# Kernel optimization log

Hardware: AMD Instinct MI355X
Metric: run time of the kernel (lower is better)

Reference implementation:

```python
import jax, jax.numpy as jnp
import numpy as np

B, N, M = 16, 4096, 1024
INPUT_DIM, COND_DIM = 512, 512
HEADS, DIM_HEAD = 8, 64
HIDDEN = HEADS * DIM_HEAD


def setup_inputs() -> dict:
    key = jax.random.key(0)
    ks = jax.random.split(key, 6)
    x = jax.random.normal(ks[0], (B, INPUT_DIM, N), dtype=jnp.float32)
    c = jax.random.normal(ks[1], (B, COND_DIM, M), dtype=jnp.float32)
    # 1x1 conv weights as [out_ch, in_ch] matrices
    Wq = jax.random.normal(ks[2], (HIDDEN, INPUT_DIM), dtype=jnp.float32) * (INPUT_DIM ** -0.5)
    Wkv = jax.random.normal(ks[3], (2 * HIDDEN, COND_DIM), dtype=jnp.float32) * (COND_DIM ** -0.5)
    Wo = jax.random.normal(ks[4], (INPUT_DIM, HIDDEN), dtype=jnp.float32) * (HIDDEN ** -0.5)
    bo = jax.random.normal(ks[5], (INPUT_DIM,), dtype=jnp.float32) * 0.01
    return {"x": x, "c": c, "Wq": Wq, "Wkv": Wkv, "Wo": Wo, "bo": bo}


def reference(x, c, Wq, Wkv, Wo, bo):
    scale = DIM_HEAD ** -0.5
    # 1x1 convs == channel-mixing matmuls
    q = jnp.einsum('bcn,oc->bon', x, Wq)            # [B, HIDDEN, N]
    kv = jnp.einsum('bcm,oc->bom', c, Wkv)          # [B, 2*HIDDEN, M]
    k, v = jnp.split(kv, 2, axis=1)                 # each [B, HIDDEN, M]
    # split heads: b (h d) n -> b h d n
    q = q.reshape(B, HEADS, DIM_HEAD, N) * scale
    k = k.reshape(B, HEADS, DIM_HEAD, M)
    v = v.reshape(B, HEADS, DIM_HEAD, M)
    # softmax over conditioning sequence dim
    k = jax.nn.softmax(k, axis=-1)
    # context: [B, H, d, e] (dim_head x dim_head)
    context = jnp.einsum('bhdm,bhem->bhde', k, v)
    # out: [B, H, e, N]
    out = jnp.einsum('bhde,bhdn->bhen', context, q)
    out = out.reshape(B, HIDDEN, N)
    return jnp.einsum('bcn,oc->bon', out, Wo) + bo[None, :, None]
```

## Files before the change

kernel.cpp:

```cpp
#include <hip/hip_runtime.h>

#define KDIM 512

typedef __attribute__((ext_vector_type(8))) short bf16x8;
typedef __attribute__((ext_vector_type(4))) float f32x4;
typedef unsigned short u16;
typedef unsigned int u32;

static __device__ __forceinline__ u16 f2bf(float f) {
  u32 u = __builtin_bit_cast(u32, f);
  u32 r = u + 0x7fffu + ((u >> 16) & 1u);
  return (u16)(r >> 16);
}
static __device__ __forceinline__ bf16x8 ld_frag(const u16* p) {
  uint2 lo = *(const uint2*)p;
  uint2 hi = *(const uint2*)(p + 4);
  uint4 u = make_uint4(lo.x, lo.y, hi.x, hi.y);
  return __builtin_bit_cast(bf16x8, u);
}

__global__ __launch_bounds__(256) void cvt_f32_bf16(
    const float* __restrict__ src, u16* __restrict__ dst, int n8)
{
  int i = blockIdx.x * 256 + threadIdx.x;
  if (i >= n8) return;
  float4 a = *(const float4*)(src + (long)i * 8);
  float4 b = *(const float4*)(src + (long)i * 8 + 4);
  u32 w0 = (u32)f2bf(a.x) | ((u32)f2bf(a.y) << 16);
  u32 w1 = (u32)f2bf(a.z) | ((u32)f2bf(a.w) << 16);
  u32 w2 = (u32)f2bf(b.x) | ((u32)f2bf(b.y) << 16);
  u32 w3 = (u32)f2bf(b.z) | ((u32)f2bf(b.w) << 16);
  *(uint4*)(dst + (long)i * 8) = make_uint4(w0, w1, w2, w3);
}

#define A0OFF 0
#define A1OFF 18432
#define B0OFF 36864
#define B1OFF 41472

#define P_LOADA(pa, kt) { _Pragma("unroll") \
  for (int i_ = 0; i_ < 4; ++i_) \
    pa[i_] = *(const uint4*)(Ab + (long)(arow + i_ * 128) * KDIM + (kt) + ac * 8); }

#define P_LOADB(q0, q1, kt) { \
  q0 = *(const float4*)(Bb + (long)((kt) + krow)     * ldn + nq * 4); \
  q1 = *(const float4*)(Bb + (long)((kt) + krow + 1) * ldn + nq * 4); }

#define P_STAGE(pa, q0, q1, ab, bb) { \
  _Pragma("unroll") for (int i_ = 0; i_ < 4; ++i_) { \
    u16* d_ = &lds[(ab) + (arow + i_ * 128) * 36 + ac * 8]; \
    *(uint2*)d_       = make_uint2(pa[i_].x, pa[i_].y); \
    *(uint2*)(d_ + 4) = make_uint2(pa[i_].z, pa[i_].w); } \
  float f0_[4] = {q0.x, q0.y, q0.z, q0.w}; \
  float f1_[4] = {q1.x, q1.y, q1.z, q1.w}; \
  _Pragma("unroll") for (int j_ = 0; j_ < 4; ++j_) { \
    u32 w_ = (u32)f2bf(f0_[j_]) | ((u32)f2bf(f1_[j_]) << 16); \
    *(u32*)&lds[(bb) + (nq * 4 + j_) * 36 + krow] = w_; } }

#define P_MFMA(ab, bb) { \
  bf16x8 bfr_[4]; \
  _Pragma("unroll") for (int ni_ = 0; ni_ < 4; ++ni_) \
    bfr_[ni_] = ld_frag(&lds[(bb) + (wn * 64 + ni_ * 16 + lrow) * 36 + lkh * 8]); \
  __builtin_amdgcn_s_setprio(1); \
  _Pragma("unroll") for (int mi_ = 0; mi_ < 8; ++mi_) { \
    bf16x8 af_ = ld_frag(&lds[(ab) + (wm * 128 + mi_ * 16 + lrow) * 36 + lkh * 8]); \
    _Pragma("unroll") for (int ni_ = 0; ni_ < 4; ++ni_) \
      acc[mi_][ni_] = __builtin_amdgcn_mfma_f32_16x16x32_bf16(af_, bfr_[ni_], acc[mi_][ni_], 0, 0, 0); } \
  __builtin_amdgcn_s_setprio(0); }

template<bool OUT_BF16, bool BIAS, int MT, int NT>
__global__ __launch_bounds__(512, 2) void gemm_p(
    const u16* __restrict__ Ap, long a_bstride,
    const float* __restrict__ Bp, long b_bstride,
    void* __restrict__ Op, long o_bstride,
    const float* __restrict__ bias, int ldn)
{
  __shared__ u16 lds[46080];

  const int d = blockIdx.x;
  const int mt = d % MT;
  const int nt = (d / MT) % NT;
  const int b  = d / (MT * NT);
  const long mtile = (long)mt * 512;
  const long ntile = (long)nt * 128;
  const u16* Ab = Ap + (long)b * a_bstride + mtile * KDIM;
  const float* Bb = Bp + (long)b * b_bstride + ntile;

  const int t = threadIdx.x;
  const int lane = t & 63, wv = t >> 6;
  const int wm = wv >> 1, wn = wv & 1;
  const int lrow = lane & 15, lkh = lane >> 4;

  const int arow = t >> 2, ac = t & 3;
  const int nq = t & 31;
  const int hi = (t >> 8) & 1;
  const int kq = ((t >> 5) & 7) ^ ((t >> 2) & 7);
  const int krow = kq * 4 + hi * 2;

  f32x4 acc[8][4] = {};
  uint4 pa0[4], pa1[4];
  float4 b0a, b0b, b1a, b1b;

  P_LOADA(pa0, 0)  P_LOADB(b0a, b0b, 0)
  P_LOADA(pa1, 32) P_LOADB(b1a, b1b, 32)
  P_STAGE(pa0, b0a, b0b, A0OFF, B0OFF)
  __syncthreads();

  for (int s2 = 0; s2 < 8; ++s2) {
    const int kt = s2 * 64;
    if (s2 < 7) { P_LOADA(pa0, kt + 64) P_LOADB(b0a, b0b, kt + 64) }
    P_MFMA(A0OFF, B0OFF)
    P_STAGE(pa1, b1a, b1b, A1OFF, B1OFF)
    __syncthreads();
    if (s2 < 7) { P_LOADA(pa1, kt + 96) P_LOADB(b1a, b1b, kt + 96) }
    P_MFMA(A1OFF, B1OFF)
    if (s2 < 7) {
      P_STAGE(pa0, b0a, b0b, A0OFF, B0OFF)
      __syncthreads();
    }
  }

  #pragma unroll
  for (int mi = 0; mi < 8; ++mi) {
    #pragma unroll
    for (int r = 0; r < 4; ++r) {
      long gr = mtile + wm * 128 + mi * 16 + lkh * 4 + r;
      float bv = 0.0f;
      if constexpr (BIAS) bv = bias[gr];
      #pragma unroll
      for (int ni = 0; ni < 4; ++ni) {
        long gc = ntile + wn * 64 + ni * 16 + lrow;
        float v = acc[mi][ni][r] + bv;
        if constexpr (OUT_BF16)
          ((u16*)Op)[(long)b * o_bstride + gr * ldn + gc] = f2bf(v);
        else
          ((float*)Op)[(long)b * o_bstride + gr * ldn + gc] = v;
      }
    }
  }
}

__global__ __launch_bounds__(256, 2) void softmax_context(
    const u16* __restrict__ kv, float* __restrict__ ctx)
{
  constexpr int LDE = 132;
  __shared__ float rowmax[64], rowinv[64];
  __shared__ u16 Ke[64 * LDE];
  __shared__ u16 Vs[64 * LDE];
  __shared__ float pr[64 * 68];

  const int bh = blockIdx.x;
  const u16* Kr = kv + (long)(bh >> 3) * (1024 * 1024) + (long)(bh & 7) * (64 * 1024);
  const u16* Vr = Kr + 512 * 1024;

  const int t = threadIdx.x;
  const int lane = t & 63, wv = t >> 6;
  const int lrow = lane & 15, lkh = lane >> 4;
  const int d4 = t >> 2, q4 = t & 3;

  {
    const u16* row = Kr + d4 * 1024 + q4 * 256;
    float mx = -3e38f;
    for (int i = 0; i < 256; i += 8) {
      uint4 v = *(const uint4*)(row + i);
      u32 ws[4] = {v.x, v.y, v.z, v.w};
      #pragma unroll
      for (int j = 0; j < 4; ++j) {
        mx = fmaxf(mx, __builtin_bit_cast(float, ws[j] << 16));
        mx = fmaxf(mx, __builtin_bit_cast(float, ws[j] & 0xffff0000u));
      }
    }
    mx = fmaxf(mx, __shfl_xor(mx, 1));
    mx = fmaxf(mx, __shfl_xor(mx, 2));
    float s = 0.f;
    for (int i = 0; i < 256; i += 8) {
      uint4 v = *(const uint4*)(row + i);
      u32 ws[4] = {v.x, v.y, v.z, v.w};
      #pragma unroll
      for (int j = 0; j < 4; ++j) {
        s += __expf(__builtin_bit_cast(float, ws[j] << 16) - mx);
        s += __expf(__builtin_bit_cast(float, ws[j] & 0xffff0000u) - mx);
      }
    }
    s += __shfl_xor(s, 1);
    s += __shfl_xor(s, 2);
    if (q4 == 0) { rowmax[d4] = mx; rowinv[d4] = 1.f / s; }
  }
  __syncthreads();

  f32x4 cacc[4][4] = {};

  for (int mc = 0; mc < 8; ++mc) {
    {
      int dd = t >> 2, j = t & 3;
      int m0 = mc * 128 + j * 32;
      float mx = rowmax[dd], inv = rowinv[dd];
      const u16* src = Kr + dd * 1024 + m0;
      u16* dst = &Ke[dd * LDE + j * 32];
      #pragma unroll
      for (int cq = 0; cq < 4; ++cq) {
        uint4 v = *(const uint4*)(src + cq * 8);
        u32 in[4] = {v.x, v.y, v.z, v.w};
        u32 out[4];
        #pragma unroll
        for (int j2 = 0; j2 < 4; ++j2) {
          float lo = __builtin_bit_cast(float, in[j2] << 16);
          float hif = __builtin_bit_cast(float, in[j2] & 0xffff0000u);
          out[j2] = (u32)f2bf(__expf(lo - mx) * inv) |
                    ((u32)f2bf(__expf(hif - mx) * inv) << 16);
        }
        *(uint2*)(dst + cq * 8)     = make_uint2(out[0], out[1]);
        *(uint2*)(dst + cq * 8 + 4) = make_uint2(out[2], out[3]);
      }
      const u16* vsrc = Vr + dd * 1024 + m0;
      u16* vdst = &Vs[dd * LDE + j * 32];
      #pragma unroll
      for (int cq = 0; cq < 4; ++cq) {
        uint4 v = *(const uint4*)(vsrc + cq * 8);
        *(uint2*)(vdst + cq * 8)     = make_uint2(v.x, v.y);
        *(uint2*)(vdst + cq * 8 + 4) = make_uint2(v.z, v.w);
      }
    }
    __syncthreads();
    bf16x8 ka[4], vb[4];
    #pragma unroll
    for (int mi = 0; mi < 4; ++mi)
      ka[mi] = ld_frag(&Ke[(mi * 16 + lrow) * LDE + wv * 32 + lkh * 8]);
    #pragma unroll
    for (int ni = 0; ni < 4; ++ni)
      vb[ni] = ld_frag(&Vs[(ni * 16 + lrow) * LDE + wv * 32 + lkh * 8]);
    #pragma unroll
    for (int mi = 0; mi < 4; ++mi)
      #pragma unroll
      for (int ni = 0; ni < 4; ++ni)
        cacc[mi][ni] = __builtin_amdgcn_mfma_f32_16x16x32_bf16(ka[mi], vb[ni], cacc[mi][ni], 0, 0, 0);
    __syncthreads();
  }

  for (int w = 0; w < 4; ++w) {
    if (wv == w) {
      #pragma unroll
      for (int mi = 0; mi < 4; ++mi)
        #pragma unroll
        for (int ni = 0; ni < 4; ++ni)
          #pragma unroll
          for (int r = 0; r < 4; ++r) {
            float* p = &pr[(mi * 16 + lkh * 4 + r) * 68 + (ni * 16 + lrow)];
            float v = cacc[mi][ni][r];
            if (w == 0) *p = v; else *p += v;
          }
    }
    __syncthreads();
  }
  float* cg = ctx + (long)bh * 4096;
  for (int i = 0; i < 16; ++i) {
    int o = t + i * 256;
    cg[o] = 0.125f * pr[(o >> 6) * 68 + (o & 63)];
  }
}

__global__ __launch_bounds__(256) void compose_u(
    const float* __restrict__ ctx, const float* __restrict__ Wo, u16* __restrict__ U)
{
  __shared__ float cs[16 * 64];
  const int bh = blockIdx.x, dq = blockIdx.y;
  const int b = bh >> 3, h = bh & 7;
  const int t = threadIdx.x;
  const float* cgrp = ctx + (long)bh * 4096 + dq * 16 * 64;
  for (int i = t; i < 1024; i += 256) cs[i] = cgrp[i];
  __syncthreads();
  #pragma unroll
  for (int rep = 0; rep < 2; ++rep) {
    int o = rep * 256 + t;
    const float* wrow = Wo + (long)o * 512 + h * 64;
    float acc[16] = {};
    for (int e = 0; e < 64; ++e) {
      float w = wrow[e];
      #pragma unroll
      for (int dd = 0; dd < 16; ++dd) acc[dd] += w * cs[dd * 64 + e];
    }
    u16* urow = U + (long)b * (512 * 512) + (long)o * 512 + h * 64 + dq * 16;
    #pragma unroll
    for (int dd = 0; dd < 16; ++dd) urow[dd] = f2bf(acc[dd]);
  }
}

extern "C" void kernel_launch(void* const* d_in, const int* in_sizes, int n_in,
                              void* d_out, int out_size, void* d_ws, size_t ws_size,
                              hipStream_t stream)
{
  const float* x   = (const float*)d_in[0];
  const float* c   = (const float*)d_in[1];
  const float* Wq  = (const float*)d_in[2];
  const float* Wkv = (const float*)d_in[3];
  const float* Wo  = (const float*)d_in[4];
  const float* bo  = (const float*)d_in[5];

  char* ws = (char*)d_ws;
  u16*   kv   = (u16*)ws;
  float* ctx  = (float*)(ws + 33554432);
  u16*   U    = (u16*)(ws + 35651584);
  u16*   Weff = (u16*)(ws + 44040192);
  u16*   Wkvb = (u16*)(ws + 44040192);

  cvt_f32_bf16<<<dim3(256), 256, 0, stream>>>(Wkv, Wkvb, 65536);
  gemm_p<true, false, 2, 8><<<dim3(2 * 8 * 16), 512, 0, stream>>>(
      Wkvb, 0, c, 512L * 1024, kv, 1024L * 1024, nullptr, 1024);
  softmax_context<<<dim3(128), 256, 0, stream>>>(kv, ctx);
  compose_u<<<dim3(128, 4), 256, 0, stream>>>(ctx, Wo, U);
  gemm_p<true, false, 1, 4><<<dim3(1 * 4 * 16), 512, 0, stream>>>(
      U, 512L * 512, Wq, 0, Weff, 512L * 512, nullptr, 512);
  gemm_p<false, true, 1, 32><<<dim3(1 * 32 * 16), 512, 0, stream>>>(
      Weff, 512L * 512, x, 512L * 4096, d_out, 512L * 4096, bo, 4096);
}
```

Measured before the change: 176.2 us.

## Deepen GEMM global-load prefetch to four B stages with fully unrolled K loop

Replaces the two-stage K loop in the GEMM with sixteen fully unrolled steps. B (fp32 activation) loads are now issued four K-chunks ahead in registers, and A loads three ahead, to hide global memory latency. The A tile's LDS row stride goes from 36 to 40 elements so A stores and fragment loads can use single 128-bit accesses. This costs more registers and more LDS, which may reduce occupancy or cause spills under the 512x2 launch bounds.

```diff
diff --git a/kernel.cpp b/kernel.cpp
--- a/kernel.cpp
+++ b/kernel.cpp
@@ -34,48 +34,59 @@
 }
 
 #define A0OFF 0
-#define A1OFF 18432
-#define B0OFF 36864
-#define B1OFF 41472
-
-#define P_LOADA(pa, kt) { _Pragma("unroll") \
+#define A1OFF 20480
+#define B0OFF 40960
+#define B1OFF 45568
+
+#define R_LOADA(set, kt) { _Pragma("unroll") \
   for (int i_ = 0; i_ < 4; ++i_) \
-    pa[i_] = *(const uint4*)(Ab + (long)(arow + i_ * 128) * KDIM + (kt) + ac * 8); }
-
-#define P_LOADB(q0, q1, kt) { \
-  q0 = *(const float4*)(Bb + (long)((kt) + krow)     * ldn + nq * 4); \
-  q1 = *(const float4*)(Bb + (long)((kt) + krow + 1) * ldn + nq * 4); }
-
-#define P_STAGE(pa, q0, q1, ab, bb) { \
-  _Pragma("unroll") for (int i_ = 0; i_ < 4; ++i_) { \
-    u16* d_ = &lds[(ab) + (arow + i_ * 128) * 36 + ac * 8]; \
-    *(uint2*)d_       = make_uint2(pa[i_].x, pa[i_].y); \
-    *(uint2*)(d_ + 4) = make_uint2(pa[i_].z, pa[i_].w); } \
-  float f0_[4] = {q0.x, q0.y, q0.z, q0.w}; \
-  float f1_[4] = {q1.x, q1.y, q1.z, q1.w}; \
+    pa##set[i_] = *(const uint4*)(Ab + (long)(arow + i_ * 128) * KDIM + (kt) + ac * 8); }
+
+#define R_LOADB(set, kt) { \
+  pb##set##a = *(const float4*)(Bb + (long)((kt) + krow)     * ldn + nq * 4); \
+  pb##set##b = *(const float4*)(Bb + (long)((kt) + krow + 1) * ldn + nq * 4); }
+
+#define R_STAGE(aset, bset, ab, bb) { \
+  _Pragma("unroll") for (int i_ = 0; i_ < 4; ++i_) \
+    *(uint4*)&lds[(ab) + (arow + i_ * 128) * 40 + ac * 8] = pa##aset[i_]; \
+  float f0_[4] = {pb##bset##a.x, pb##bset##a.y, pb##bset##a.z, pb##bset##a.w}; \
+  float f1_[4] = {pb##bset##b.x, pb##bset##b.y, pb##bset##b.z, pb##bset##b.w}; \
   _Pragma("unroll") for (int j_ = 0; j_ < 4; ++j_) { \
     u32 w_ = (u32)f2bf(f0_[j_]) | ((u32)f2bf(f1_[j_]) << 16); \
     *(u32*)&lds[(bb) + (nq * 4 + j_) * 36 + krow] = w_; } }
 
-#define P_MFMA(ab, bb) { \
+#define R_MFMA(ab, bb) { \
   bf16x8 bfr_[4]; \
   _Pragma("unroll") for (int ni_ = 0; ni_ < 4; ++ni_) \
     bfr_[ni_] = ld_frag(&lds[(bb) + (wn * 64 + ni_ * 16 + lrow) * 36 + lkh * 8]); \
   __builtin_amdgcn_s_setprio(1); \
   _Pragma("unroll") for (int mi_ = 0; mi_ < 8; ++mi_) { \
-    bf16x8 af_ = ld_frag(&lds[(ab) + (wm * 128 + mi_ * 16 + lrow) * 36 + lkh * 8]); \
+    bf16x8 af_ = *(const bf16x8*)&lds[(ab) + (wm * 128 + mi_ * 16 + lrow) * 40 + lkh * 8]; \
     _Pragma("unroll") for (int ni_ = 0; ni_ < 4; ++ni_) \
       acc[mi_][ni_] = __builtin_amdgcn_mfma_f32_16x16x32_bf16(af_, bfr_[ni_], acc[mi_][ni_], 0, 0, 0); } \
   __builtin_amdgcn_s_setprio(0); }
 
+#define R_STEP(s, a0, a1, b0, b1, b2, b3) { \
+  constexpr int ab_  = ((s) & 1) ? A1OFF : A0OFF; \
+  constexpr int bb_  = ((s) & 1) ? B1OFF : B0OFF; \
+  constexpr int abn_ = ((s) & 1) ? A0OFF : A1OFF; \
+  constexpr int bbn_ = ((s) & 1) ? B0OFF : B1OFF; \
+  if constexpr ((s) < 12) { R_LOADB(b0, ((s) + 4) * 32) } \
+  R_MFMA(ab_, bb_) \
+  if constexpr ((s) < 15) { \
+    R_STAGE(a1, b1, abn_, bbn_) \
+    if constexpr ((s) < 13) { R_LOADA(a1, ((s) + 3) * 32) } \
+    __syncthreads(); \
+  } }
+
 template<bool OUT_BF16, bool BIAS, int MT, int NT>
-__global__ __launch_bounds__(512, 2) void gemm_p(
+__global__ __launch_bounds__(512, 2) void gemm_r(
     const u16* __restrict__ Ap, long a_bstride,
     const float* __restrict__ Bp, long b_bstride,
     void* __restrict__ Op, long o_bstride,
     const float* __restrict__ bias, int ldn)
 {
-  __shared__ u16 lds[46080];
+  __shared__ u16 lds[50176];
 
   const int d = blockIdx.x;
   const int mt = d % MT;
@@ -99,26 +110,30 @@
 
   f32x4 acc[8][4] = {};
   uint4 pa0[4], pa1[4];
-  float4 b0a, b0b, b1a, b1b;
-
-  P_LOADA(pa0, 0)  P_LOADB(b0a, b0b, 0)
-  P_LOADA(pa1, 32) P_LOADB(b1a, b1b, 32)
-  P_STAGE(pa0, b0a, b0b, A0OFF, B0OFF)
+  float4 pb0a, pb0b, pb1a, pb1b, pb2a, pb2b, pb3a, pb3b;
+
+  R_LOADB(0, 0) R_LOADB(1, 32) R_LOADB(2, 64) R_LOADB(3, 96)
+  R_LOADA(0, 0) R_LOADA(1, 32)
+  R_STAGE(0, 0, A0OFF, B0OFF)
+  R_LOADA(0, 64)
   __syncthreads();
 
-  for (int s2 = 0; s2 < 8; ++s2) {
-    const int kt = s2 * 64;
-    if (s2 < 7) { P_LOADA(pa0, kt + 64) P_LOADB(b0a, b0b, kt + 64) }
-    P_MFMA(A0OFF, B0OFF)
-    P_STAGE(pa1, b1a, b1b, A1OFF, B1OFF)
-    __syncthreads();
-    if (s2 < 7) { P_LOADA(pa1, kt + 96) P_LOADB(b1a, b1b, kt + 96) }
-    P_MFMA(A1OFF, B1OFF)
-    if (s2 < 7) {
-      P_STAGE(pa0, b0a, b0b, A0OFF, B0OFF)
-      __syncthreads();
-    }
-  }
+  R_STEP(0,  0, 1, 0, 1, 2, 3)
+  R_STEP(1,  1, 0, 1, 2, 3, 0)
+  R_STEP(2,  0, 1, 2, 3, 0, 1)
+  R_STEP(3,  1, 0, 3, 0, 1, 2)
+  R_STEP(4,  0, 1, 0, 1, 2, 3)
+  R_STEP(5,  1, 0, 1, 2, 3, 0)
+  R_STEP(6,  0, 1, 2, 3, 0, 1)
+  R_STEP(7,  1, 0, 3, 0, 1, 2)
+  R_STEP(8,  0, 1, 0, 1, 2, 3)
+  R_STEP(9,  1, 0, 1, 2, 3, 0)
+  R_STEP(10, 0, 1, 2, 3, 0, 1)
+  R_STEP(11, 1, 0, 3, 0, 1, 2)
+  R_STEP(12, 0, 1, 0, 1, 2, 3)
+  R_STEP(13, 1, 0, 1, 2, 3, 0)
+  R_STEP(14, 0, 1, 2, 3, 0, 1)
+  R_STEP(15, 1, 0, 3, 0, 1, 2)
 
   #pragma unroll
   for (int mi = 0; mi < 8; ++mi) {
@@ -304,12 +319,12 @@
   u16*   Wkvb = (u16*)(ws + 44040192);
 
   cvt_f32_bf16<<<dim3(256), 256, 0, stream>>>(Wkv, Wkvb, 65536);
-  gemm_p<true, false, 2, 8><<<dim3(2 * 8 * 16), 512, 0, stream>>>(
+  gemm_r<true, false, 2, 8><<<dim3(2 * 8 * 16), 512, 0, stream>>>(
       Wkvb, 0, c, 512L * 1024, kv, 1024L * 1024, nullptr, 1024);
   softmax_context<<<dim3(128), 256, 0, stream>>>(kv, ctx);
   compose_u<<<dim3(128, 4), 256, 0, stream>>>(ctx, Wo, U);
-  gemm_p<true, false, 1, 4><<<dim3(1 * 4 * 16), 512, 0, stream>>>(
+  gemm_r<true, false, 1, 4><<<dim3(1 * 4 * 16), 512, 0, stream>>>(
       U, 512L * 512, Wq, 0, Weff, 512L * 512, nullptr, 512);
-  gemm_p<false, true, 1, 32><<<dim3(1 * 32 * 16), 512, 0, stream>>>(
+  gemm_r<false, true, 1, 32><<<dim3(1 * 32 * 16), 512, 0, stream>>>(
       Weff, 512L * 512, x, 512L * 4096, d_out, 512L * 4096, bo, 4096);
 }
```

Result: slower. 274.5 us (+55.8%).

## Load GEMM A tiles directly into LDS with async global_load_lds and XOR swizzle

Applied to the files above, without the earlier changes.

Replaces the register-staged A-operand path in the shared bf16 GEMM with global_load_lds direct-to-LDS transfers, using an unpadded 32-element row layout with an XOR swizzle to avoid bank conflicts on fragment reads. This removes the register round-trip and LDS write instructions for A, frees registers, and shrinks the LDS footprint. B still goes through registers for fp32-to-bf16 conversion. The pipeline is reordered so each half-stage issues its loads just before the MFMA on the other buffer. That ordering relies on the barrier placement to cover completion of the asynchronous LDS writes.

```diff
diff --git a/kernel.cpp b/kernel.cpp
--- a/kernel.cpp
+++ b/kernel.cpp
@@ -18,6 +18,11 @@
   uint4 u = make_uint4(lo.x, lo.y, hi.x, hi.y);
   return __builtin_bit_cast(bf16x8, u);
 }
+
+#define GLOADLDS(g, l) \
+  __builtin_amdgcn_global_load_lds( \
+      (const __attribute__((address_space(1))) void*)(g), \
+      (__attribute__((address_space(3))) void*)(l), 16, 0, 0)
 
 __global__ __launch_bounds__(256) void cvt_f32_bf16(
     const float* __restrict__ src, u16* __restrict__ dst, int n8)
@@ -34,48 +39,48 @@
 }
 
 #define A0OFF 0
-#define A1OFF 18432
-#define B0OFF 36864
-#define B1OFF 41472
-
-#define P_LOADA(pa, kt) { _Pragma("unroll") \
-  for (int i_ = 0; i_ < 4; ++i_) \
-    pa[i_] = *(const uint4*)(Ab + (long)(arow + i_ * 128) * KDIM + (kt) + ac * 8); }
-
-#define P_LOADB(q0, q1, kt) { \
-  q0 = *(const float4*)(Bb + (long)((kt) + krow)     * ldn + nq * 4); \
-  q1 = *(const float4*)(Bb + (long)((kt) + krow + 1) * ldn + nq * 4); }
-
-#define P_STAGE(pa, q0, q1, ab, bb) { \
-  _Pragma("unroll") for (int i_ = 0; i_ < 4; ++i_) { \
-    u16* d_ = &lds[(ab) + (arow + i_ * 128) * 36 + ac * 8]; \
-    *(uint2*)d_       = make_uint2(pa[i_].x, pa[i_].y); \
-    *(uint2*)(d_ + 4) = make_uint2(pa[i_].z, pa[i_].w); } \
-  float f0_[4] = {q0.x, q0.y, q0.z, q0.w}; \
-  float f1_[4] = {q1.x, q1.y, q1.z, q1.w}; \
+#define A1OFF 16384
+#define B0OFF 32768
+#define B1OFF 37376
+
+#define T_GLOADA(kt, ab) { _Pragma("unroll") \
+  for (int i_ = 0; i_ < 4; ++i_) { \
+    int r_ = (i_ * 8 + wv) * 16 + (lane >> 2); \
+    int g_ = (lane & 3) ^ ((r_ >> 2) & 3); \
+    GLOADLDS(Ab + (long)r_ * KDIM + (kt) + g_ * 8, \
+             &lds[(ab) + (i_ * 8 + wv) * 512]); } }
+
+#define T_LOADB(set, kt) { \
+  pb##set##a = *(const float4*)(Bb + (long)((kt) + krow)     * ldn + nq * 4); \
+  pb##set##b = *(const float4*)(Bb + (long)((kt) + krow + 1) * ldn + nq * 4); }
+
+#define T_STAGEB(set, bb) { \
+  float f0_[4] = {pb##set##a.x, pb##set##a.y, pb##set##a.z, pb##set##a.w}; \
+  float f1_[4] = {pb##set##b.x, pb##set##b.y, pb##set##b.z, pb##set##b.w}; \
   _Pragma("unroll") for (int j_ = 0; j_ < 4; ++j_) { \
     u32 w_ = (u32)f2bf(f0_[j_]) | ((u32)f2bf(f1_[j_]) << 16); \
     *(u32*)&lds[(bb) + (nq * 4 + j_) * 36 + krow] = w_; } }
 
-#define P_MFMA(ab, bb) { \
+#define T_MFMA(ab, bb) { \
   bf16x8 bfr_[4]; \
   _Pragma("unroll") for (int ni_ = 0; ni_ < 4; ++ni_) \
     bfr_[ni_] = ld_frag(&lds[(bb) + (wn * 64 + ni_ * 16 + lrow) * 36 + lkh * 8]); \
   __builtin_amdgcn_s_setprio(1); \
   _Pragma("unroll") for (int mi_ = 0; mi_ < 8; ++mi_) { \
-    bf16x8 af_ = ld_frag(&lds[(ab) + (wm * 128 + mi_ * 16 + lrow) * 36 + lkh * 8]); \
+    int r_ = wm * 128 + mi_ * 16 + lrow; \
+    bf16x8 af_ = *(const bf16x8*)&lds[(ab) + r_ * 32 + arsel]; \
     _Pragma("unroll") for (int ni_ = 0; ni_ < 4; ++ni_) \
       acc[mi_][ni_] = __builtin_amdgcn_mfma_f32_16x16x32_bf16(af_, bfr_[ni_], acc[mi_][ni_], 0, 0, 0); } \
   __builtin_amdgcn_s_setprio(0); }
 
 template<bool OUT_BF16, bool BIAS, int MT, int NT>
-__global__ __launch_bounds__(512, 2) void gemm_p(
+__global__ __launch_bounds__(512, 2) void gemm_t(
     const u16* __restrict__ Ap, long a_bstride,
     const float* __restrict__ Bp, long b_bstride,
     void* __restrict__ Op, long o_bstride,
     const float* __restrict__ bias, int ldn)
 {
-  __shared__ u16 lds[46080];
+  __shared__ u16 lds[41984];
 
   const int d = blockIdx.x;
   const int mt = d % MT;
@@ -90,32 +95,35 @@
   const int lane = t & 63, wv = t >> 6;
   const int wm = wv >> 1, wn = wv & 1;
   const int lrow = lane & 15, lkh = lane >> 4;
-
-  const int arow = t >> 2, ac = t & 3;
+  const int arsel = (lkh ^ ((lrow >> 2) & 3)) * 8;
+
   const int nq = t & 31;
   const int hi = (t >> 8) & 1;
   const int kq = ((t >> 5) & 7) ^ ((t >> 2) & 7);
   const int krow = kq * 4 + hi * 2;
 
   f32x4 acc[8][4] = {};
-  uint4 pa0[4], pa1[4];
-  float4 b0a, b0b, b1a, b1b;
-
-  P_LOADA(pa0, 0)  P_LOADB(b0a, b0b, 0)
-  P_LOADA(pa1, 32) P_LOADB(b1a, b1b, 32)
-  P_STAGE(pa0, b0a, b0b, A0OFF, B0OFF)
+  float4 pb0a, pb0b, pb1a, pb1b;
+
+  T_LOADB(0, 0)
+  T_GLOADA(0, A0OFF)
+  T_STAGEB(0, B0OFF)
   __syncthreads();
 
   for (int s2 = 0; s2 < 8; ++s2) {
     const int kt = s2 * 64;
-    if (s2 < 7) { P_LOADA(pa0, kt + 64) P_LOADB(b0a, b0b, kt + 64) }
-    P_MFMA(A0OFF, B0OFF)
-    P_STAGE(pa1, b1a, b1b, A1OFF, B1OFF)
+    T_LOADB(1, kt + 32)
+    T_GLOADA(kt + 32, A1OFF)
+    T_MFMA(A0OFF, B0OFF)
+    T_STAGEB(1, B1OFF)
     __syncthreads();
-    if (s2 < 7) { P_LOADA(pa1, kt + 96) P_LOADB(b1a, b1b, kt + 96) }
-    P_MFMA(A1OFF, B1OFF)
     if (s2 < 7) {
-      P_STAGE(pa0, b0a, b0b, A0OFF, B0OFF)
+      T_LOADB(0, kt + 64)
+      T_GLOADA(kt + 64, A0OFF)
+    }
+    T_MFMA(A1OFF, B1OFF)
+    if (s2 < 7) {
+      T_STAGEB(0, B0OFF)
       __syncthreads();
     }
   }
@@ -304,12 +312,12 @@
   u16*   Wkvb = (u16*)(ws + 44040192);
 
   cvt_f32_bf16<<<dim3(256), 256, 0, stream>>>(Wkv, Wkvb, 65536);
-  gemm_p<true, false, 2, 8><<<dim3(2 * 8 * 16), 512, 0, stream>>>(
+  gemm_t<true, false, 2, 8><<<dim3(2 * 8 * 16), 512, 0, stream>>>(
       Wkvb, 0, c, 512L * 1024, kv, 1024L * 1024, nullptr, 1024);
   softmax_context<<<dim3(128), 256, 0, stream>>>(kv, ctx);
   compose_u<<<dim3(128, 4), 256, 0, stream>>>(ctx, Wo, U);
-  gemm_p<true, false, 1, 4><<<dim3(1 * 4 * 16), 512, 0, stream>>>(
+  gemm_t<true, false, 1, 4><<<dim3(1 * 4 * 16), 512, 0, stream>>>(
       U, 512L * 512, Wq, 0, Weff, 512L * 512, nullptr, 512);
-  gemm_p<false, true, 1, 32><<<dim3(1 * 32 * 16), 512, 0, stream>>>(
+  gemm_t<false, true, 1, 32><<<dim3(1 * 32 * 16), 512, 0, stream>>>(
       Weff, 512L * 512, x, 512L * 4096, d_out, 512L * 4096, bo, 4096);
 }
```

Measured after the change: 213.1 us. 20.9% more time.
